# Optimization experiments

Measured on AMD Instinct MI355X. Metric: run time of the kernel, lower is better.

Reference implementation:

```python
import jax, jax.numpy as jnp
import numpy as np

TS = 16      # tile size
ST = 4       # stride
IN = 224     # image size
G = (IN - TS) // ST + 1   # 53 tiles per side
L = G * G                 # 2809 tiles
CH = [3 * L, 3 * L // 4, 3 * L // 16, 3 * L // 4, 3 * L]  # [8427,2106,526,2106,8427]

# torch_dct-style unnormalized DCT-II matrix and its exact inverse (DCT-III based)
_n = np.arange(TS)
_k = np.arange(TS)[:, None]
_C = np.cos(np.pi * (2 * _n[None, :] + 1) * _k / (2 * TS))  # [k, n]
D_DCT = jnp.asarray(2.0 * _C, jnp.float32)                   # dct: y = D @ x
_w = np.ones(TS); _w[0] = 0.5
D_IDCT = jnp.asarray((_C.T * _w[None, :]) / TS, jnp.float32) # idct: x = Dinv @ y

# gather/scatter indices for unfold/fold (constants)
IH = (np.arange(G) * ST)[:, None] + np.arange(TS)[None, :]   # [G, TS]
IW = IH


def setup_inputs() -> dict:
    key = jax.random.key(0)
    ks = jax.random.split(key, 9)
    x = jax.random.normal(ks[0], (8, 3, IN, IN), jnp.float32)
    def lin(k, o, c):
        return jax.random.normal(k, (o, c), jnp.float32) * 0.02
    return {
        'x': x,
        'w1': lin(ks[1], CH[1], CH[0]), 'b1': jnp.zeros((CH[1],), jnp.float32),
        'w2': lin(ks[2], CH[2], CH[1]), 'b2': jnp.zeros((CH[2],), jnp.float32),
        'w3': lin(ks[3], CH[3], CH[2]), 'b3': jnp.zeros((CH[3],), jnp.float32),
        'w4': lin(ks[4], CH[4], CH[3]), 'b4': jnp.zeros((CH[4],), jnp.float32),
    }


def _forward(x, w1, b1, w2, b2, w3, b3, w4, b4):
    b = x.shape[0]
    # unfold: gather overlapping 16x16 patches -> [b, 3, G, G, TS, TS]
    p = x[:, :, IH[:, None, :, None], IW[None, :, None, :]]
    # torch ordering after permute+reshape: channel index = l*3 + c
    tiles = p.transpose(0, 2, 3, 1, 4, 5).reshape(b, 3 * L, TS, TS)
    # 2D DCT (unnormalized DCT-II along last two dims)
    dct_tiles = jnp.einsum('km,ln,bcmn->bckl', D_DCT, D_DCT, tiles)
    # mask net: stack of 1x1 convs over the tile-channel dim
    h = dct_tiles / (TS * TS)
    h = jax.nn.relu(jnp.einsum('oc,bchw->bohw', w1, h) + b1[:, None, None])
    h = jax.nn.relu(jnp.einsum('oc,bchw->bohw', w2, h) + b2[:, None, None])
    h = jax.nn.relu(jnp.einsum('oc,bchw->bohw', w3, h) + b3[:, None, None])
    masks = jax.nn.sigmoid(jnp.einsum('oc,bchw->bohw', w4, h) + b4[:, None, None])
    clean_dct = masks * dct_tiles
    # 2D inverse DCT
    clean_tiles = jnp.einsum('mk,nl,bckl->bcmn', D_IDCT, D_IDCT, clean_dct)
    # fold: scatter-add patches back with overlap
    ct = clean_tiles.reshape(b, G, G, 3, TS, TS).transpose(0, 3, 1, 2, 4, 5)
    out = jnp.zeros((b, 3, IN, IN), x.dtype)
    out = out.at[:, :, IH[:, None, :, None], IW[None, :, None, :]].add(ct)
    # scale = fold(unfold(ones)): per-pixel overlap counts (recomputed per call, as in source)
    scale = jnp.zeros((IN, IN), x.dtype)
    scale = scale.at[IH[:, None, :, None], IW[None, :, None, :]].add(
        jnp.ones((G, G, TS, TS), x.dtype))
    return out / scale


def reference(x, w1, b1, w2, b2, w3, b3, w4, b4):
    return _forward(x, w1, b1, w2, b2, w3, b3, w4, b4)
```

## Files before the change

kernel.cpp:

```cpp
#include <hip/hip_runtime.h>
#include <stdint.h>

constexpr int INSZ = 224;
constexpr int GD   = 53;
constexpr int C0R = 8427, C1R = 2106, C2R = 526;
constexpr int C0P = 8448, C1P = 2304, C2P = 640;
constexpr int NTOK = 2048;

typedef __attribute__((ext_vector_type(4))) float f32x4;
typedef __attribute__((ext_vector_type(8))) short bf16x8;

constexpr float CT[64] = {
  1.00000000f,  0.99518473f,  0.98078528f,  0.95694034f,
  0.92387953f,  0.88192126f,  0.83146961f,  0.77301045f,
  0.70710678f,  0.63439328f,  0.55557023f,  0.47139674f,
  0.38268343f,  0.29028468f,  0.19509032f,  0.09801714f,
  0.00000000f, -0.09801714f, -0.19509032f, -0.29028468f,
 -0.38268343f, -0.47139674f, -0.55557023f, -0.63439328f,
 -0.70710678f, -0.77301045f, -0.83146961f, -0.88192126f,
 -0.92387953f, -0.95694034f, -0.98078528f, -0.99518473f,
 -1.00000000f, -0.99518473f, -0.98078528f, -0.95694034f,
 -0.92387953f, -0.88192126f, -0.83146961f, -0.77301045f,
 -0.70710678f, -0.63439328f, -0.55557023f, -0.47139674f,
 -0.38268343f, -0.29028468f, -0.19509032f, -0.09801714f,
 -0.00000000f,  0.09801714f,  0.19509032f,  0.29028468f,
  0.38268343f,  0.47139674f,  0.55557023f,  0.63439328f,
  0.70710678f,  0.77301045f,  0.83146961f,  0.88192126f,
  0.92387953f,  0.95694034f,  0.98078528f,  0.99518473f
};
constexpr float Dfwd(int k, int n) { return 2.0f * CT[((2 * n + 1) * k) & 63]; }
constexpr float Dinv(int n, int k) { return CT[((2 * n + 1) * k) & 63] * (k == 0 ? 0.03125f : 0.0625f); }

constexpr int TRS_R = 20, TRS_T = 336;
constexpr int TRS_SZ = 15 * TRS_T + 15 * TRS_R + 16;

__device__ __forceinline__ unsigned short f2bf(float f) {
  union { float f; unsigned u; } v; v.f = f;
  return (unsigned short)((v.u + 0x7FFFu + ((v.u >> 16) & 1u)) >> 16);
}
__device__ __forceinline__ float bf2f(unsigned short b) {
  union { unsigned u; float f; } v; v.u = ((unsigned)b) << 16;
  return v.f;
}

__device__ __forceinline__ void gload_lds16(const void* g, void* l) {
  __builtin_amdgcn_global_load_lds(
      (__attribute__((address_space(1))) unsigned int*)(uintptr_t)g,
      (__attribute__((address_space(3))) unsigned int*)(unsigned int)(uintptr_t)l,
      16, 0, 0);
}

__device__ __forceinline__ void xcd_tile(int& bx, int& by) {
  const int gx = gridDim.x, gy = gridDim.y;
  const int nwg = gx * gy;
  const int bid = blockIdx.y * gx + blockIdx.x;
  const int cpx = nwg >> 3;
  const int l = (bid & 7) * cpx + (bid >> 3);
  const int stripe = gy << 2;
  const int bxg = l / stripe;
  const int r = l - bxg * stripe;
  const int rem = gx - (bxg << 2);
  const int w = rem < 4 ? rem : 4;
  by = r / w;
  bx = (bxg << 2) + (r - by * w);
}

__global__ void cvt_pad(const float* __restrict__ src, unsigned short* __restrict__ dst,
                        int M, int K, int Kp) {
  const int k = blockIdx.x * 256 + threadIdx.x;
  const int m = blockIdx.y;
  if (k >= Kp) return;
  const float v = (m < M && k < K) ? src[(size_t)m * K + k] : 0.f;
  dst[(size_t)m * Kp + k] = f2bf(v);
}

constexpr int CVA1 = C2P * C1P;
constexpr int CVA2 = CVA1 + C1P * C2P;
constexpr int CVTOT = CVA2 + C0P * C1P;
__global__ void cvt_pad_all(const float* __restrict__ w2, const float* __restrict__ w3,
                            const float* __restrict__ w4, unsigned short* __restrict__ d2,
                            unsigned short* __restrict__ d3, unsigned short* __restrict__ d4) {
  const int i = blockIdx.x * 256 + threadIdx.x;
  if (i < CVA1) {
    const int m = i / C1P, k = i - m * C1P;
    d2[i] = f2bf((m < C2R && k < C1R) ? w2[(size_t)m * C1R + k] : 0.f);
  } else if (i < CVA2) {
    const int j = i - CVA1;
    const int m = j / C2P, k = j - m * C2P;
    d3[j] = f2bf((m < C1R && k < C2R) ? w3[(size_t)m * C2R + k] : 0.f);
  } else {
    const int j = i - CVA2;
    const int m = j / C1P, k = j - m * C1P;
    d4[j] = f2bf((m < C0R && k < C1R) ? w4[(size_t)m * C1R + k] : 0.f);
  }
}

__global__ __launch_bounds__(256)
void dct_h0(const float* __restrict__ x, unsigned short* __restrict__ H0) {
  __shared__ float trp[TRS_SZ];
  __shared__ unsigned short hst[256 * 64];
  const int tid = threadIdx.x;
  const int b   = blockIdx.y;
  const int c0  = blockIdx.x * 64;
  const int t = tid >> 4, q = tid & 15;

  for (int g = 0; g < 4; ++g) {
    const int c = c0 + g * 16 + t;
    float p[16];
    {
      float4 v0{}, v1{}, v2{}, v3{};
      if (c < C0R) {
        const int ch = c % 3, gw = (c / 3) % GD, gh = c / (3 * GD);
        const float* xr = x + ((size_t)(b * 3 + ch) * INSZ + (gh * 4 + q)) * INSZ + gw * 4;
        v0 = *(const float4*)(xr);      v1 = *(const float4*)(xr + 4);
        v2 = *(const float4*)(xr + 8);  v3 = *(const float4*)(xr + 12);
      }
      p[0]=v0.x; p[1]=v0.y; p[2]=v0.z; p[3]=v0.w;
      p[4]=v1.x; p[5]=v1.y; p[6]=v1.z; p[7]=v1.w;
      p[8]=v2.x; p[9]=v2.y; p[10]=v2.z; p[11]=v2.w;
      p[12]=v3.x; p[13]=v3.y; p[14]=v3.z; p[15]=v3.w;
    }
    float r[16];
#pragma unroll
    for (int k = 0; k < 16; ++k) {
      float s = 0.f;
#pragma unroll
      for (int n = 0; n < 16; ++n) s += p[n] * Dfwd(k, n);
      r[k] = s;
    }
    float* wr = &trp[t * TRS_T + q * TRS_R];
#pragma unroll
    for (int k = 0; k < 16; k += 4)
      *(float4*)(wr + k) = make_float4(r[k], r[k+1], r[k+2], r[k+3]);
    __syncthreads();
    const int j = q;
    float rr[16];
#pragma unroll
    for (int i = 0; i < 16; ++i) rr[i] = trp[t * TRS_T + i * TRS_R + j];
#pragma unroll
    for (int k = 0; k < 16; ++k) {
      float s = 0.f;
#pragma unroll
      for (int i = 0; i < 16; ++i) s += rr[i] * Dfwd(k, i);
      hst[(k * 16 + j) * 64 + g * 16 + t] = f2bf(s * (1.f / 256.f));
    }
    __syncthreads();
  }
  const size_t base = ((size_t)b * 256) * C0P + c0;
#pragma unroll
  for (int i = 0; i < 8; ++i) {
    const int s = i * 256 + tid;
    const int kl = s >> 3, c16 = s & 7;
    *(uint4*)&H0[base + (size_t)kl * C0P + c16 * 8] = *(const uint4*)&hst[kl * 64 + c16 * 8];
  }
}

template<int ACT, int OUT_NM, int SPLITK>
__global__ __launch_bounds__(512, 2)
void gemm256(const unsigned short* __restrict__ W, const unsigned short* __restrict__ Ht,
             const float* __restrict__ bias, void* __restrict__ outp,
             int ldo, int Kp, int chunkK) {
  __shared__ unsigned short As[3][8192];
  __shared__ unsigned short Bs[3][8192];
  int bx, by; xcd_tile(bx, by);
  const int m0 = bx * 256, n0 = by * 256;
  const int tid = threadIdx.x;
  const int w = tid >> 6, lane = tid & 63;
  const int wr = w >> 2, wc = w & 3;
  const int lhi = lane >> 4, llo = lane & 15;
  const int kbase = SPLITK ? blockIdx.z * chunkK : 0;
  const int nkt = chunkK >> 5;

  const int srow = tid >> 2;
  const int slgc = ((tid & 3) ^ ((srow >> 1) & 3)) * 8;

  f32x4 acc[8][4];
#pragma unroll
  for (int i = 0; i < 8; ++i)
#pragma unroll
    for (int j = 0; j < 4; ++j) acc[i][j] = f32x4{0.f, 0.f, 0.f, 0.f};

  auto STAGE_A = [&](int kt, int buf) {
    const int kb = kbase + kt * 32 + slgc;
    gload_lds16(W + (size_t)(m0 + srow) * Kp + kb,       &As[buf][w * 512]);
    gload_lds16(W + (size_t)(m0 + 128 + srow) * Kp + kb, &As[buf][4096 + w * 512]);
  };
  auto STAGE_B = [&](int kt, int buf) {
    const int kb = kbase + kt * 32 + slgc;
    gload_lds16(Ht + (size_t)(n0 + srow) * Kp + kb,       &Bs[buf][w * 512]);
    gload_lds16(Ht + (size_t)(n0 + 128 + srow) * Kp + kb, &Bs[buf][4096 + w * 512]);
  };

  STAGE_A(0, 0); STAGE_B(0, 0);
  if (nkt > 1) { STAGE_A(1, 1); STAGE_B(1, 1); }

  int buf = 0;
  for (int kt = 0; kt < nkt; ++kt) {
    const int sbuf = buf >= 1 ? buf - 1 : 2;
    if (kt + 1 < nkt) asm volatile("s_waitcnt vmcnt(4)" ::: "memory");
    else              asm volatile("s_waitcnt vmcnt(0)" ::: "memory");
    __builtin_amdgcn_s_barrier();
    __builtin_amdgcn_sched_barrier(0);

    bf16x8 af[4], bfr[4];
#pragma unroll
    for (int mi = 0; mi < 4; ++mi) {
      const int row = wr * 128 + mi * 16 + llo;
      af[mi] = *(const bf16x8*)(&As[buf][row * 32 + ((lhi ^ ((row >> 1) & 3)) << 3)]);
    }
#pragma unroll
    for (int ni = 0; ni < 4; ++ni) {
      const int row = wc * 64 + ni * 16 + llo;
      bfr[ni] = *(const bf16x8*)(&Bs[buf][row * 32 + ((lhi ^ ((row >> 1) & 3)) << 3)]);
    }
    if (kt + 2 < nkt) STAGE_A(kt + 2, sbuf);
    __builtin_amdgcn_s_setprio(1);
#pragma unroll
    for (int mi = 0; mi < 4; ++mi)
#pragma unroll
      for (int ni = 0; ni < 4; ++ni)
        acc[mi][ni] = OUT_NM
          ? __builtin_amdgcn_mfma_f32_16x16x32_bf16(bfr[ni], af[mi], acc[mi][ni], 0, 0, 0)
          : __builtin_amdgcn_mfma_f32_16x16x32_bf16(af[mi], bfr[ni], acc[mi][ni], 0, 0, 0);
    __builtin_amdgcn_s_setprio(0);
    __builtin_amdgcn_s_barrier();
    __builtin_amdgcn_sched_barrier(0);
#pragma unroll
    for (int mi = 0; mi < 4; ++mi) {
      const int row = wr * 128 + 64 + mi * 16 + llo;
      af[mi] = *(const bf16x8*)(&As[buf][row * 32 + ((lhi ^ ((row >> 1) & 3)) << 3)]);
    }
    if (kt + 2 < nkt) STAGE_B(kt + 2, sbuf);
    __builtin_amdgcn_s_setprio(1);
#pragma unroll
    for (int mi = 0; mi < 4; ++mi)
#pragma unroll
      for (int ni = 0; ni < 4; ++ni)
        acc[4 + mi][ni] = OUT_NM
          ? __builtin_amdgcn_mfma_f32_16x16x32_bf16(bfr[ni], af[mi], acc[4 + mi][ni], 0, 0, 0)
          : __builtin_amdgcn_mfma_f32_16x16x32_bf16(af[mi], bfr[ni], acc[4 + mi][ni], 0, 0, 0);
    __builtin_amdgcn_s_setprio(0);
    buf = buf == 2 ? 0 : buf + 1;
  }

  if (SPLITK) {
    float* pz = (float*)outp + (size_t)blockIdx.z * ((size_t)NTOK * ldo);
#pragma unroll
    for (int mh = 0; mh < 2; ++mh)
#pragma unroll
      for (int mi = 0; mi < 4; ++mi) {
        const int mg = m0 + wr * 128 + mh * 64 + mi * 16 + llo;
#pragma unroll
        for (int ni = 0; ni < 4; ++ni) {
          const int ng = n0 + wc * 64 + ni * 16 + lhi * 4;
#pragma unroll
          for (int r = 0; r < 4; ++r)
            pz[(size_t)(ng + r) * ldo + mg] = acc[mh * 4 + mi][ni][r];
        }
      }
  } else {
    unsigned short* out = (unsigned short*)outp;
#pragma unroll
    for (int mh = 0; mh < 2; ++mh)
#pragma unroll
      for (int mi = 0; mi < 4; ++mi) {
        const int mgb = m0 + wr * 128 + mh * 64 + mi * 16 + lhi * 4;
#pragma unroll
        for (int ni = 0; ni < 4; ++ni) {
          const int ng = n0 + wc * 64 + ni * 16 + llo;
#pragma unroll
          for (int r = 0; r < 4; ++r) {
            const int mg = mgb + r;
            float v = acc[mh * 4 + mi][ni][r] + bias[mg];
            if (ACT == 1) v = fmaxf(v, 0.f);
            else if (ACT == 2) v = 1.f / (1.f + expf(-v));
            out[(size_t)mg * ldo + ng] = f2bf(v);
          }
        }
      }
  }
}

template<int OUT_NM>
__device__ __forceinline__ void gemm_core(
    const unsigned short* __restrict__ W, const unsigned short* __restrict__ Ht,
    unsigned short (*As)[128 * 32], unsigned short (*Bs)[128 * 32],
    int m0, int n0, int Kp, int kbase, int nkt, int w, int lane, f32x4 acc[4][4]) {
  const int wr = w >> 1, wc = w & 1;
  const int lhi = lane >> 4, llo = lane & 15;

  const int chunk0 = w * 64 + lane;
  const int row0 = chunk0 >> 2, kc0 = chunk0 & 3;
  const int kcg0 = kc0 ^ ((row0 >> 1) & 3);
  const int chunk1 = 256 + w * 64 + lane;
  const int row1 = chunk1 >> 2, kc1 = chunk1 & 3;
  const int kcg1 = kc1 ^ ((row1 >> 1) & 3);

  auto STAGE = [&](int kt, int sel) {
    const int kb = kbase + kt * 32;
    gload_lds16(W  + (size_t)(m0 + row0) * Kp + kb + kcg0 * 8, &As[sel][(w * 64) * 8]);
    gload_lds16(Ht + (size_t)(n0 + row0) * Kp + kb + kcg0 * 8, &Bs[sel][(w * 64) * 8]);
    gload_lds16(W  + (size_t)(m0 + row1) * Kp + kb + kcg1 * 8, &As[sel][(256 + w * 64) * 8]);
    gload_lds16(Ht + (size_t)(n0 + row1) * Kp + kb + kcg1 * 8, &Bs[sel][(256 + w * 64) * 8]);
  };

  STAGE(0, 0);
  if (nkt > 1) STAGE(1, 1);

  int cur = 0, nxt = 1, nx2 = 2;
  for (int kt = 0; kt < nkt; ++kt) {
    if (kt + 1 < nkt) {
      asm volatile("s_waitcnt vmcnt(4)" ::: "memory");
      __builtin_amdgcn_s_barrier();
      __builtin_amdgcn_sched_barrier(0);
      if (kt + 2 < nkt) STAGE(kt + 2, nx2);
    } else {
      asm volatile("s_waitcnt vmcnt(0)" ::: "memory");
      __builtin_amdgcn_s_barrier();
      __builtin_amdgcn_sched_barrier(0);
    }
    bf16x8 af[4], bfr[4];
#pragma unroll
    for (int mi = 0; mi < 4; ++mi) {
      const int row = wr * 64 + mi * 16 + llo;
      af[mi] = *(const bf16x8*)(&As[cur][row * 32 + (lhi ^ ((row >> 1) & 3)) * 8]);
    }
#pragma unroll
    for (int ni = 0; ni < 4; ++ni) {
      const int row = wc * 64 + ni * 16 + llo;
      bfr[ni] = *(const bf16x8*)(&Bs[cur][row * 32 + (lhi ^ ((row >> 1) & 3)) * 8]);
    }
#pragma unroll
    for (int mi = 0; mi < 4; ++mi)
#pragma unroll
      for (int ni = 0; ni < 4; ++ni) {
        if (OUT_NM)
          acc[mi][ni] = __builtin_amdgcn_mfma_f32_16x16x32_bf16(bfr[ni], af[mi], acc[mi][ni], 0, 0, 0);
        else
          acc[mi][ni] = __builtin_amdgcn_mfma_f32_16x16x32_bf16(af[mi], bfr[ni], acc[mi][ni], 0, 0, 0);
      }
    const int tmp = cur; cur = nxt; nxt = nx2; nx2 = tmp;
  }
}

template<int ACT, int OUT_NM>
__global__ __launch_bounds__(256)
void gemm_bt(const unsigned short* __restrict__ W, const unsigned short* __restrict__ Ht,
             const float* __restrict__ bias, int Mreal,
             unsigned short* __restrict__ out, int ldo, int Kp) {
  __shared__ unsigned short As[3][128 * 32];
  __shared__ unsigned short Bs[3][128 * 32];
  int bx, by; xcd_tile(bx, by);
  const int tid = threadIdx.x;
  const int w = tid >> 6, lane = tid & 63;
  const int m0 = bx * 128, n0 = by * 128;
  const int wr = w >> 1, wc = w & 1;
  const int lhi = lane >> 4, llo = lane & 15;

  f32x4 acc[4][4];
#pragma unroll
  for (int i = 0; i < 4; ++i)
#pragma unroll
    for (int j = 0; j < 4; ++j) acc[i][j] = f32x4{0.f, 0.f, 0.f, 0.f};

  gemm_core<OUT_NM>(W, Ht, As, Bs, m0, n0, Kp, 0, Kp >> 5, w, lane, acc);

  if (OUT_NM) {
#pragma unroll
    for (int mi = 0; mi < 4; ++mi) {
      const int mg = m0 + wr * 64 + mi * 16 + llo;
      const float bv = (mg < Mreal) ? bias[mg] : 0.f;
#pragma unroll
      for (int ni = 0; ni < 4; ++ni) {
        const int ng = n0 + wc * 64 + ni * 16 + lhi * 4;
#pragma unroll
        for (int r = 0; r < 4; ++r) {
          float v = acc[mi][ni][r] + bv;
          if (ACT == 1) v = fmaxf(v, 0.f);
          else if (ACT == 2) v = 1.f / (1.f + expf(-v));
          out[(size_t)(ng + r) * ldo + mg] = f2bf(v);
        }
      }
    }
  } else {
#pragma unroll
    for (int mi = 0; mi < 4; ++mi) {
      const int mgb = m0 + wr * 64 + mi * 16 + lhi * 4;
#pragma unroll
      for (int ni = 0; ni < 4; ++ni) {
        const int ng = n0 + wc * 64 + ni * 16 + llo;
#pragma unroll
        for (int r = 0; r < 4; ++r) {
          const int mg = mgb + r;
          float v = acc[mi][ni][r] + ((mg < Mreal) ? bias[mg] : 0.f);
          if (ACT == 1) v = fmaxf(v, 0.f);
          else if (ACT == 2) v = 1.f / (1.f + expf(-v));
          out[(size_t)mg * ldo + ng] = f2bf(v);
        }
      }
    }
  }
}

__global__ __launch_bounds__(256)
void gemm_splitk(const unsigned short* __restrict__ W, const unsigned short* __restrict__ Ht,
                 float* __restrict__ part, int ldo , int Kp, int chunkK) {
  __shared__ unsigned short As[3][128 * 32];
  __shared__ unsigned short Bs[3][128 * 32];
  int bx, by; xcd_tile(bx, by);
  const int z = blockIdx.z;
  const int tid = threadIdx.x;
  const int w = tid >> 6, lane = tid & 63;
  const int m0 = bx * 128, n0 = by * 128;
  const int wr = w >> 1, wc = w & 1;
  const int lhi = lane >> 4, llo = lane & 15;

  f32x4 acc[4][4];
#pragma unroll
  for (int i = 0; i < 4; ++i)
#pragma unroll
    for (int j = 0; j < 4; ++j) acc[i][j] = f32x4{0.f, 0.f, 0.f, 0.f};

  gemm_core<1>(W, Ht, As, Bs, m0, n0, Kp, z * chunkK, chunkK >> 5, w, lane, acc);

  float* pz = part + (size_t)z * NTOK * ldo;
#pragma unroll
  for (int mi = 0; mi < 4; ++mi) {
    const int mg = m0 + wr * 64 + mi * 16 + llo;
#pragma unroll
    for (int ni = 0; ni < 4; ++ni) {
      const int ng = n0 + wc * 64 + ni * 16 + lhi * 4;
#pragma unroll
      for (int r = 0; r < 4; ++r)
        pz[(size_t)(ng + r) * ldo + mg] = acc[mi][ni][r];
    }
  }
}

__global__ __launch_bounds__(256)
void reduce_act(const float* __restrict__ part, const float* __restrict__ bias,
                unsigned short* __restrict__ out, int Mp, int Mreal, int nch) {
  const int i4 = blockIdx.x * 256 + threadIdx.x;
  const int total = NTOK * Mp / 4;
  if (i4 >= total) return;
  const size_t off = (size_t)i4 * 4;
  const int m0 = (int)(off % Mp);
  float s0 = 0.f, s1 = 0.f, s2 = 0.f, s3 = 0.f;
  for (int z = 0; z < nch; ++z) {
    const float4 v = *(const float4*)(part + (size_t)z * NTOK * Mp + off);
    s0 += v.x; s1 += v.y; s2 += v.z; s3 += v.w;
  }
  s0 += (m0 + 0 < Mreal) ? bias[m0 + 0] : 0.f;
  s1 += (m0 + 1 < Mreal) ? bias[m0 + 1] : 0.f;
  s2 += (m0 + 2 < Mreal) ? bias[m0 + 2] : 0.f;
  s3 += (m0 + 3 < Mreal) ? bias[m0 + 3] : 0.f;
  s0 = fmaxf(s0, 0.f); s1 = fmaxf(s1, 0.f); s2 = fmaxf(s2, 0.f); s3 = fmaxf(s3, 0.f);
  uint2 pk;
  pk.x = (unsigned)f2bf(s0) | ((unsigned)f2bf(s1) << 16);
  pk.y = (unsigned)f2bf(s2) | ((unsigned)f2bf(s3) << 16);
  *(uint2*)&out[off] = pk;
}

__global__ __launch_bounds__(256)
void mask_idct(const float* __restrict__ x, const unsigned short* __restrict__ masks,
               unsigned short* __restrict__ clean) {
  __shared__ float trp[TRS_SZ];
  const int tid = threadIdx.x;
  const int b   = blockIdx.y;
  const int c0  = blockIdx.x * 16;
  const int t = tid >> 4, q = tid & 15;
  const int c = c0 + t;
  const bool valid = (c < C0R);

  float p[16];
  {
    float4 v0{}, v1{}, v2{}, v3{};
    if (valid) {
      const int ch = c % 3, gw = (c / 3) % GD, gh = c / (3 * GD);
      const float* xr = x + ((size_t)(b * 3 + ch) * INSZ + (gh * 4 + q)) * INSZ + gw * 4;
      v0 = *(const float4*)(xr);      v1 = *(const float4*)(xr + 4);
      v2 = *(const float4*)(xr + 8);  v3 = *(const float4*)(xr + 12);
    }
    p[0]=v0.x; p[1]=v0.y; p[2]=v0.z; p[3]=v0.w;
    p[4]=v1.x; p[5]=v1.y; p[6]=v1.z; p[7]=v1.w;
    p[8]=v2.x; p[9]=v2.y; p[10]=v2.z; p[11]=v2.w;
    p[12]=v3.x; p[13]=v3.y; p[14]=v3.z; p[15]=v3.w;
  }
  float r[16];
#pragma unroll
  for (int k = 0; k < 16; ++k) {
    float s = 0.f;
#pragma unroll
    for (int n = 0; n < 16; ++n) s += p[n] * Dfwd(k, n);
    r[k] = s;
  }
  {
    float* wr = &trp[t * TRS_T + q * TRS_R];
#pragma unroll
    for (int k = 0; k < 16; k += 4)
      *(float4*)(wr + k) = make_float4(r[k], r[k+1], r[k+2], r[k+3]);
  }
  __syncthreads();
  const int j = q;
  float rr[16];
#pragma unroll
  for (int i = 0; i < 16; ++i) rr[i] = trp[t * TRS_T + i * TRS_R + j];
  float cd[16];
  const unsigned short* mrow = masks + (size_t)c * NTOK + (size_t)b * 256 + j;
#pragma unroll
  for (int k = 0; k < 16; ++k) {
    float s = 0.f;
#pragma unroll
    for (int i = 0; i < 16; ++i) s += rr[i] * Dfwd(k, i);
    const float mv = valid ? bf2f(mrow[k * 16]) : 0.f;
    cd[k] = s * mv;
  }
  float t3[16];
#pragma unroll
  for (int m = 0; m < 16; ++m) {
    float s = 0.f;
#pragma unroll
    for (int k = 0; k < 16; ++k) s += cd[k] * Dinv(m, k);
    t3[m] = s;
  }
  __syncthreads();
  {
    float* wr = &trp[t * TRS_T + j * TRS_R];
#pragma unroll
    for (int m = 0; m < 16; m += 4)
      *(float4*)(wr + m) = make_float4(t3[m], t3[m+1], t3[m+2], t3[m+3]);
  }
  __syncthreads();
  float tr[16];
#pragma unroll
  for (int l = 0; l < 16; ++l) tr[l] = trp[t * TRS_T + l * TRS_R + q];
  if (valid) {
    unsigned pk[8];
#pragma unroll
    for (int n2 = 0; n2 < 8; ++n2) {
      float s0 = 0.f, s1 = 0.f;
#pragma unroll
      for (int l = 0; l < 16; ++l) {
        s0 += tr[l] * Dinv(2 * n2, l);
        s1 += tr[l] * Dinv(2 * n2 + 1, l);
      }
      pk[n2] = (unsigned)f2bf(s0) | ((unsigned)f2bf(s1) << 16);
    }
    unsigned short* dst = clean + ((size_t)b * C0R + c) * 256 + q * 16;
    uint4* d4 = (uint4*)dst;
    d4[0] = make_uint4(pk[0], pk[1], pk[2], pk[3]);
    d4[1] = make_uint4(pk[4], pk[5], pk[6], pk[7]);
  }
}

__global__ void overlap_add(const unsigned short* __restrict__ clean, float* __restrict__ out) {
  const int px = blockIdx.x * 256 + threadIdx.x;
  if (px >= 8 * 3 * 224 * 224) return;
  const int j = px % 224;
  const int i = (px / 224) % 224;
  const int bc = px / (224 * 224);
  const int ch = bc % 3, b = bc / 3;
  const int ilo = i - 15;
  const int ghlo = ilo > 0 ? (ilo + 3) >> 2 : 0;
  const int ghhi = (i >> 2) < 52 ? (i >> 2) : 52;
  const int jlo = j - 15;
  const int gwlo = jlo > 0 ? (jlo + 3) >> 2 : 0;
  const int gwhi = (j >> 2) < 52 ? (j >> 2) : 52;
  float sum = 0.f;
  for (int gh = ghlo; gh <= ghhi; ++gh) {
    const int r = i - gh * 4;
    const size_t base = ((size_t)b * C0R + (size_t)gh * (3 * GD) + ch) * 256 + (size_t)r * 16 + j;
    for (int gw = gwlo; gw <= gwhi; ++gw) {
      sum += bf2f(clean[base + (size_t)gw * 764]);
    }
  }
  const int cnt = (ghhi - ghlo + 1) * (gwhi - gwlo + 1);
  out[px] = sum / (float)cnt;
}

extern "C" void kernel_launch(void* const* d_in, const int* in_sizes, int n_in,
                              void* d_out, int out_size, void* d_ws, size_t ws_size,
                              hipStream_t stream) {
  const float* x  = (const float*)d_in[0];
  const float* w1 = (const float*)d_in[1];
  const float* b1 = (const float*)d_in[2];
  const float* w2 = (const float*)d_in[3];
  const float* b2 = (const float*)d_in[4];
  const float* w3 = (const float*)d_in[5];
  const float* b3 = (const float*)d_in[6];
  const float* w4 = (const float*)d_in[7];
  const float* b4 = (const float*)d_in[8];
  float* out = (float*)d_out;
  char* ws = (char*)d_ws;

  const size_t OFF_A = 0;
  const size_t OFF_B = 38928384;
  const size_t OFF_C = 73531392;

  unsigned short* wb1   = (unsigned short*)(ws + OFF_A);
  unsigned short* wb4   = (unsigned short*)(ws + OFF_A);
  unsigned short* clean = (unsigned short*)(ws + OFF_A);

  unsigned short* H0v = (unsigned short*)(ws + OFF_B);
  unsigned short* Y1  = (unsigned short*)(ws + OFF_B);
  unsigned short* wb2 = (unsigned short*)(ws + OFF_B + 9437184);
  unsigned short* wb3 = (unsigned short*)(ws + OFF_B + 12386304);
  unsigned short* Y2  = (unsigned short*)(ws + OFF_B + 15335424);
  unsigned short* msk = (unsigned short*)(ws + OFF_B);

  float* pt1 = (float*)(ws + OFF_C);
  float* pt2 = (float*)(ws + OFF_C);
  float* pt3 = (float*)(ws + OFF_C);
  unsigned short* Y3 = (unsigned short*)(ws + OFF_C + 37748736);

  cvt_pad<<<dim3((C0P + 255) / 256, C1P), 256, 0, stream>>>(w1, wb1, C1R, C0R, C0P);
  dct_h0<<<dim3(C0P / 64, 8), 256, 0, stream>>>(x, H0v);

  gemm256<0, 1, 1><<<dim3(C1P / 256, NTOK / 256, 3), 512, 0, stream>>>(
      wb1, H0v, nullptr, pt1, C1P, C0P, 2816);
  reduce_act<<<dim3(NTOK * C1P / 4 / 256), 256, 0, stream>>>(pt1, b1, Y1, C1P, C1R, 3);

  cvt_pad_all<<<dim3(CVTOT / 256), 256, 0, stream>>>(w2, w3, w4, wb2, wb3, wb4);

  gemm_splitk<<<dim3(C2P / 128, NTOK / 128, 4), 256, 0, stream>>>(wb2, Y1, pt2, C2P, C1P, 576);
  reduce_act<<<dim3(NTOK * C2P / 4 / 256), 256, 0, stream>>>(pt2, b2, Y2, C2P, C2R, 4);

  gemm_splitk<<<dim3(C1P / 128, NTOK / 128, 2), 256, 0, stream>>>(wb3, Y2, pt3, C1P, C2P, 320);
  reduce_act<<<dim3(NTOK * C1P / 4 / 256), 256, 0, stream>>>(pt3, b3, Y3, C1P, C1R, 2);

  gemm256<2, 0, 0><<<dim3(32, NTOK / 256), 512, 0, stream>>>(
      wb4, Y3, b4, msk, NTOK, C1P, C1P);
  gemm_bt<2, 0><<<dim3(2, NTOK / 128), 256, 0, stream>>>(
      wb4 + (size_t)8192 * C1P, Y3, b4 + 8192, C0R - 8192,
      msk + (size_t)8192 * NTOK, NTOK, C1P);

  mask_idct<<<dim3((C0R + 15) / 16, 8), 256, 0, stream>>>(x, msk, clean);

  overlap_add<<<dim3((8 * 3 * 224 * 224 + 255) / 256), 256, 0, stream>>>(clean, out);
}
```

Baseline: 434.4 us.

## Deepen gemm256 LDS pipeline to four stages and vectorize weight bf16 conversion

The gemm256 kernel moves from a 3-buffer to a 4-buffer LDS ring, prefetching three K-tiles ahead with adjusted vmcnt waits so global-load latency is hidden better. The weight fp32-to-bf16 pad/convert kernels now handle 8 elements per thread and write 16-byte packed stores instead of one scalar store per thread. LDS use per block grows from 96KB to 128KB, which may break the 2-blocks-per-CU occupancy that launch_bounds(512,2) targets.

Result: no change. 428.9 us (-1.3%).

```diff
diff --git a/kernel.cpp b/kernel.cpp
--- a/kernel.cpp
+++ b/kernel.cpp
@@ -65,34 +65,65 @@
   bx = (bxg << 2) + (r - by * w);
 }
 
-__global__ void cvt_pad(const float* __restrict__ src, unsigned short* __restrict__ dst,
-                        int M, int K, int Kp) {
-  const int k = blockIdx.x * 256 + threadIdx.x;
-  const int m = blockIdx.y;
-  if (k >= Kp) return;
-  const float v = (m < M && k < K) ? src[(size_t)m * K + k] : 0.f;
-  dst[(size_t)m * Kp + k] = f2bf(v);
-}
-
-constexpr int CVA1 = C2P * C1P;
-constexpr int CVA2 = CVA1 + C1P * C2P;
-constexpr int CVTOT = CVA2 + C0P * C1P;
-__global__ void cvt_pad_all(const float* __restrict__ w2, const float* __restrict__ w3,
-                            const float* __restrict__ w4, unsigned short* __restrict__ d2,
-                            unsigned short* __restrict__ d3, unsigned short* __restrict__ d4) {
+constexpr int CV1_GPR = C0P / 8;
+constexpr int CV1_TOT = C1P * CV1_GPR;
+__global__ __launch_bounds__(256)
+void cvt_pad8_w1(const float* __restrict__ src, unsigned short* __restrict__ dst) {
   const int i = blockIdx.x * 256 + threadIdx.x;
-  if (i < CVA1) {
-    const int m = i / C1P, k = i - m * C1P;
-    d2[i] = f2bf((m < C2R && k < C1R) ? w2[(size_t)m * C1R + k] : 0.f);
-  } else if (i < CVA2) {
-    const int j = i - CVA1;
-    const int m = j / C2P, k = j - m * C2P;
-    d3[j] = f2bf((m < C1R && k < C2R) ? w3[(size_t)m * C2R + k] : 0.f);
+  if (i >= CV1_TOT) return;
+  const int m = i / CV1_GPR;
+  const int k0 = (i - m * CV1_GPR) * 8;
+  const float* sr = src + (size_t)m * C0R + k0;
+  const bool mok = (m < C1R);
+  unsigned short h[8];
+#pragma unroll
+  for (int e = 0; e < 8; ++e)
+    h[e] = f2bf((mok && k0 + e < C0R) ? sr[e] : 0.f);
+  uint4 pk;
+  pk.x = (unsigned)h[0] | ((unsigned)h[1] << 16);
+  pk.y = (unsigned)h[2] | ((unsigned)h[3] << 16);
+  pk.z = (unsigned)h[4] | ((unsigned)h[5] << 16);
+  pk.w = (unsigned)h[6] | ((unsigned)h[7] << 16);
+  *(uint4*)&dst[(size_t)m * C0P + k0] = pk;
+}
+
+constexpr int CV8_1 = C2P * C1P / 8;
+constexpr int CV8_2 = CV8_1 + C1P * C2P / 8;
+constexpr int CV8_T = CV8_2 + C0P * C1P / 8;
+__global__ __launch_bounds__(256)
+void cvt_pad8_all(const float* __restrict__ w2, const float* __restrict__ w3,
+                  const float* __restrict__ w4, unsigned short* __restrict__ d2,
+                  unsigned short* __restrict__ d3, unsigned short* __restrict__ d4) {
+  const int i = blockIdx.x * 256 + threadIdx.x;
+  const float* src; unsigned short* dst;
+  int m, k0, Kreal, Mreal, Kp;
+  if (i < CV8_1) {
+    const int gpr = C1P / 8;
+    m = i / gpr; k0 = (i - m * gpr) * 8;
+    src = w2; dst = d2; Mreal = C2R; Kreal = C1R; Kp = C1P;
+  } else if (i < CV8_2) {
+    const int j = i - CV8_1;
+    const int gpr = C2P / 8;
+    m = j / gpr; k0 = (j - m * gpr) * 8;
+    src = w3; dst = d3; Mreal = C1R; Kreal = C2R; Kp = C2P;
   } else {
-    const int j = i - CVA2;
-    const int m = j / C1P, k = j - m * C1P;
-    d4[j] = f2bf((m < C0R && k < C1R) ? w4[(size_t)m * C1R + k] : 0.f);
-  }
+    const int j = i - CV8_2;
+    const int gpr = C1P / 8;
+    m = j / gpr; k0 = (j - m * gpr) * 8;
+    src = w4; dst = d4; Mreal = C0R; Kreal = C1R; Kp = C1P;
+  }
+  const float* sr = src + (size_t)m * Kreal + k0;
+  const bool mok = (m < Mreal);
+  unsigned short h[8];
+#pragma unroll
+  for (int e = 0; e < 8; ++e)
+    h[e] = f2bf((mok && k0 + e < Kreal) ? sr[e] : 0.f);
+  uint4 pk;
+  pk.x = (unsigned)h[0] | ((unsigned)h[1] << 16);
+  pk.y = (unsigned)h[2] | ((unsigned)h[3] << 16);
+  pk.z = (unsigned)h[4] | ((unsigned)h[5] << 16);
+  pk.w = (unsigned)h[6] | ((unsigned)h[7] << 16);
+  *(uint4*)&dst[(size_t)m * Kp + k0] = pk;
 }
 
 __global__ __launch_bounds__(256)
@@ -160,8 +191,8 @@
 void gemm256(const unsigned short* __restrict__ W, const unsigned short* __restrict__ Ht,
              const float* __restrict__ bias, void* __restrict__ outp,
              int ldo, int Kp, int chunkK) {
-  __shared__ unsigned short As[3][8192];
-  __shared__ unsigned short Bs[3][8192];
+  __shared__ unsigned short As[4][8192];
+  __shared__ unsigned short Bs[4][8192];
   int bx, by; xcd_tile(bx, by);
   const int m0 = bx * 256, n0 = by * 256;
   const int tid = threadIdx.x;
@@ -193,12 +224,14 @@
 
   STAGE_A(0, 0); STAGE_B(0, 0);
   if (nkt > 1) { STAGE_A(1, 1); STAGE_B(1, 1); }
-
-  int buf = 0;
+  if (nkt > 2) { STAGE_A(2, 2); STAGE_B(2, 2); }
+
   for (int kt = 0; kt < nkt; ++kt) {
-    const int sbuf = buf >= 1 ? buf - 1 : 2;
-    if (kt + 1 < nkt) asm volatile("s_waitcnt vmcnt(4)" ::: "memory");
-    else              asm volatile("s_waitcnt vmcnt(0)" ::: "memory");
+    const int buf  = kt & 3;
+    const int sbuf = (kt + 3) & 3;
+    if (kt + 3 <= nkt)      asm volatile("s_waitcnt vmcnt(8)" ::: "memory");
+    else if (kt + 2 == nkt) asm volatile("s_waitcnt vmcnt(4)" ::: "memory");
+    else                    asm volatile("s_waitcnt vmcnt(0)" ::: "memory");
     __builtin_amdgcn_s_barrier();
     __builtin_amdgcn_sched_barrier(0);
 
@@ -213,7 +246,7 @@
       const int row = wc * 64 + ni * 16 + llo;
       bfr[ni] = *(const bf16x8*)(&Bs[buf][row * 32 + ((lhi ^ ((row >> 1) & 3)) << 3)]);
     }
-    if (kt + 2 < nkt) STAGE_A(kt + 2, sbuf);
+    if (kt + 3 < nkt) STAGE_A(kt + 3, sbuf);
     __builtin_amdgcn_s_setprio(1);
 #pragma unroll
     for (int mi = 0; mi < 4; ++mi)
@@ -230,7 +263,7 @@
       const int row = wr * 128 + 64 + mi * 16 + llo;
       af[mi] = *(const bf16x8*)(&As[buf][row * 32 + ((lhi ^ ((row >> 1) & 3)) << 3)]);
     }
-    if (kt + 2 < nkt) STAGE_B(kt + 2, sbuf);
+    if (kt + 3 < nkt) STAGE_B(kt + 3, sbuf);
     __builtin_amdgcn_s_setprio(1);
 #pragma unroll
     for (int mi = 0; mi < 4; ++mi)
@@ -240,7 +273,6 @@
           ? __builtin_amdgcn_mfma_f32_16x16x32_bf16(bfr[ni], af[mi], acc[4 + mi][ni], 0, 0, 0)
           : __builtin_amdgcn_mfma_f32_16x16x32_bf16(af[mi], bfr[ni], acc[4 + mi][ni], 0, 0, 0);
     __builtin_amdgcn_s_setprio(0);
-    buf = buf == 2 ? 0 : buf + 1;
   }
 
   if (SPLITK) {
@@ -613,14 +645,14 @@
   float* pt3 = (float*)(ws + OFF_C);
   unsigned short* Y3 = (unsigned short*)(ws + OFF_C + 37748736);
 
-  cvt_pad<<<dim3((C0P + 255) / 256, C1P), 256, 0, stream>>>(w1, wb1, C1R, C0R, C0P);
+  cvt_pad8_w1<<<dim3(CV1_TOT / 256), 256, 0, stream>>>(w1, wb1);
   dct_h0<<<dim3(C0P / 64, 8), 256, 0, stream>>>(x, H0v);
 
   gemm256<0, 1, 1><<<dim3(C1P / 256, NTOK / 256, 3), 512, 0, stream>>>(
       wb1, H0v, nullptr, pt1, C1P, C0P, 2816);
   reduce_act<<<dim3(NTOK * C1P / 4 / 256), 256, 0, stream>>>(pt1, b1, Y1, C1P, C1R, 3);
 
-  cvt_pad_all<<<dim3(CVTOT / 256), 256, 0, stream>>>(w2, w3, w4, wb2, wb3, wb4);
+  cvt_pad8_all<<<dim3(CV8_T / 256), 256, 0, stream>>>(w2, w3, w4, wb2, wb3, wb4);
 
   gemm_splitk<<<dim3(C2P / 128, NTOK / 128, 4), 256, 0, stream>>>(wb2, Y1, pt2, C2P, C1P, 576);
   reduce_act<<<dim3(NTOK * C2P / 4 / 256), 256, 0, stream>>>(pt2, b2, Y2, C2P, C2R, 4);
```
